# Optimization experiments

Measured on AMD Instinct MI355X. Metric: run time of the kernel, lower is better.

The kernel has to match this reference:

```python
import jax, jax.numpy as jnp
import numpy as np

D = 1024
H = 16
HD = D // H
B = 8
S = 1024


def setup_inputs() -> dict:
    key = jax.random.key(0)
    ks = jax.random.split(key, 12)
    std = 0.02
    inp = {
        "x": jax.random.normal(ks[0], (B, S, D), jnp.float32),
        "rel_pos_enc": jax.random.normal(ks[1], (S, HD), jnp.float32) * std,
        "attention_mask": jax.random.randint(ks[2], (B, S), 0, 2, jnp.int32),
        "Wq": jax.random.normal(ks[3], (D, D), jnp.float32) * std,
        "bq": jnp.zeros((D,), jnp.float32),
        "Wk": jax.random.normal(ks[4], (D, D), jnp.float32) * std,
        "bk": jnp.zeros((D,), jnp.float32),
        "Wv": jax.random.normal(ks[5], (D, D), jnp.float32) * std,
        "bv": jnp.zeros((D,), jnp.float32),
        "Wo": jax.random.normal(ks[6], (D, D), jnp.float32) * std,
        "bo": jnp.zeros((D,), jnp.float32),
    }
    return inp


def reference(x, rel_pos_enc, attention_mask, Wq, bq, Wk, bk, Wv, bv, Wo, bo):
    b, s, d = x.shape
    scale = HD ** -0.5
    # projections + split heads -> [B, H, S, hd]
    q = (x @ Wq + bq).reshape(b, s, H, HD).transpose(0, 2, 1, 3)
    k = (x @ Wk + bk).reshape(b, s, H, HD).transpose(0, 2, 1, 3)
    v = (x @ Wv + bv).reshape(b, s, H, HD).transpose(0, 2, 1, 3)
    # content scores [B,H,S,S]
    scores = jnp.einsum("bhsd,bhtd->bhst", q, k) * scale
    # additive relative-position bias: q . rel_pos_enc[t]  -> [B,H,S,S]
    scores = scores + jnp.einsum("bhsd,td->bhst", q, rel_pos_enc)
    # key-padding mask [B,S] -> [B,1,1,S]
    scores = jnp.where(attention_mask[:, None, None, :] == 0, -jnp.inf, scores)
    attn = jax.nn.softmax(scores, axis=-1)
    ctx = jnp.einsum("bhst,bhtd->bhsd", attn, v)
    ctx = ctx.transpose(0, 2, 1, 3).reshape(b, s, d)
    return ctx @ Wo + bo
```

## Files before the change

### kernel.cpp

```cpp
#include <hip/hip_runtime.h>

#define DD 1024
#define HH 16
#define HDD 64
#define BBATCH 8
#define SS 1024
#define NROW (BBATCH*SS)
#define PSTR 72

typedef _Float16 f16x8 __attribute__((ext_vector_type(8)));
typedef _Float16 f16x4 __attribute__((ext_vector_type(4)));
typedef float    f32x4 __attribute__((ext_vector_type(4)));

__device__ __forceinline__ void async_cp16(const void* g, void* l) {
    __builtin_amdgcn_global_load_lds(
        (const __attribute__((address_space(1))) void*)g,
        (__attribute__((address_space(3))) void*)l, 16, 0, 0);
}

__global__ __launch_bounds__(256) void conv_x_kernel(
    const float* __restrict__ x, _Float16* __restrict__ xh)
{
    size_t i8 = ((size_t)blockIdx.x * 256 + threadIdx.x) * 8;
    float4 v0 = *(const float4*)&x[i8];
    float4 v1 = *(const float4*)&x[i8 + 4];
    float vf[8] = {v0.x, v0.y, v0.z, v0.w, v1.x, v1.y, v1.z, v1.w};
    f16x8 hv;
    #pragma unroll
    for (int c = 0; c < 8; c++) hv[c] = (_Float16)vf[c];
    *(f16x8*)&xh[i8] = hv;
}

__global__ __launch_bounds__(256) void conv_w_kernel(
    const float* __restrict__ Wq, const float* __restrict__ Wk,
    const float* __restrict__ Wv, const float* __restrict__ Wo,
    _Float16* __restrict__ wt, _Float16* __restrict__ wot)
{
    __shared__ float T[64][65];
    const int z = blockIdx.z;
    const float* src = (z == 0) ? Wq : (z == 1) ? Wk : (z == 2) ? Wv : Wo;
    _Float16* dh = (z < 3) ? wt + (size_t)z * 1024 * 1024 : wot;
    const int k0 = blockIdx.x * 64, n0 = blockIdx.y * 64;
    const int tid = threadIdx.x;

    #pragma unroll
    for (int rep = 0; rep < 4; rep++) {
        int e = rep * 256 + tid;
        int kr = e >> 4, nc = (e & 15) * 4;
        *(float4*)&T[kr][nc] = *(const float4*)&src[(size_t)(k0 + kr) * 1024 + n0 + nc];
    }
    __syncthreads();
    #pragma unroll
    for (int rep = 0; rep < 4; rep++) {
        int e = rep * 256 + tid;
        int nr = e >> 4, kc = (e & 15) * 4;
        f16x4 hv;
        #pragma unroll
        for (int c = 0; c < 4; c++) hv[c] = (_Float16)T[kc + c][nr];
        *(f16x4*)&dh[(size_t)(n0 + nr) * 1024 + k0 + kc] = hv;
    }
}

__global__ __launch_bounds__(256) void gemm_f16(
    const _Float16* __restrict__ Ag, const _Float16* __restrict__ Bg,
    const float* __restrict__ b0, const float* __restrict__ b1,
    const float* __restrict__ b2, const float* __restrict__ rel,
    _Float16* __restrict__ oq, _Float16* __restrict__ okh,
    _Float16* __restrict__ ovt, float* __restrict__ dOut, int mode)
{
    __shared__ _Float16 smem[32768];

    const int tid = threadIdx.x;
    const int w = tid >> 6, l = tid & 63;
    const int lane15 = l & 15, quad = l >> 4;
    const int rm = (w >> 1) * 64, cn = (w & 1) * 64;
    const size_t r0 = (size_t)blockIdx.y * 128;
    const size_t n0 = (size_t)blockIdx.x * 128;

    const int srow = tid >> 3;
    const int schp = tid & 7;
    const int sch  = schp ^ (srow & 7);

    f32x4 acc[4][4] = {};

    #pragma unroll
    for (int i = 0; i < 4; i++) {
        int row = i * 32 + srow;
        int s = row * 8 + schp;
        async_cp16(&Ag[(r0 + row) * 1024 + sch * 8], &smem[s * 8]);
        async_cp16(&Bg[(n0 + row) * 1024 + sch * 8], &smem[8192 + s * 8]);
    }
    #pragma unroll
    for (int i = 0; i < 4; i++) {
        int row = i * 32 + srow;
        int s = row * 8 + schp;
        async_cp16(&Ag[(r0 + row) * 1024 + 64 + sch * 8], &smem[16384 + s * 8]);
        async_cp16(&Bg[(n0 + row) * 1024 + 64 + sch * 8], &smem[16384 + 8192 + s * 8]);
    }

    for (int ks = 0; ks < 16; ks++) {
        const _Float16* Ah = smem + (ks & 1) * 16384;
        const _Float16* Bh = Ah + 8192;

        if (ks < 15) asm volatile("s_waitcnt vmcnt(8)" ::: "memory");
        else         asm volatile("s_waitcnt vmcnt(0)" ::: "memory");
        __builtin_amdgcn_sched_barrier(0);
        __builtin_amdgcn_s_barrier();
        __builtin_amdgcn_sched_barrier(0);

        #pragma unroll
        for (int ksub = 0; ksub < 2; ksub++) {
            f16x8 ah[4], bh4[4];
            #pragma unroll
            for (int ii = 0; ii < 4; ii++) {
                int row = rm + ii * 16 + lane15;
                int chp = (ksub * 4 + quad) ^ (row & 7);
                ah[ii] = *(const f16x8*)&Ah[row * 64 + chp * 8];
            }
            #pragma unroll
            for (int jj = 0; jj < 4; jj++) {
                int col = cn + jj * 16 + lane15;
                int chp = (ksub * 4 + quad) ^ (col & 7);
                bh4[jj] = *(const f16x8*)&Bh[col * 64 + chp * 8];
            }
            #pragma unroll
            for (int ii = 0; ii < 4; ii++)
                #pragma unroll
                for (int jj = 0; jj < 4; jj++)
                    acc[ii][jj] = __builtin_amdgcn_mfma_f32_16x16x32_f16(
                        ah[ii], bh4[jj], acc[ii][jj], 0, 0, 0);
        }

        __builtin_amdgcn_sched_barrier(0);
        __builtin_amdgcn_s_barrier();
        __builtin_amdgcn_sched_barrier(0);

        if (ks + 2 < 16) {
            const int kb = (ks + 2) * 64;
            _Float16* An = smem + (ks & 1) * 16384;
            _Float16* Bn = An + 8192;
            #pragma unroll
            for (int i = 0; i < 4; i++) {
                int row = i * 32 + srow;
                int s = row * 8 + schp;
                async_cp16(&Ag[(r0 + row) * 1024 + kb + sch * 8], &An[s * 8]);
                async_cp16(&Bg[(n0 + row) * 1024 + kb + sch * 8], &Bn[s * 8]);
            }
        }
    }

    if (mode == 0) {
        const int z = blockIdx.x >> 3;
        const float* bias = (z == 0) ? b0 : (z == 1) ? b1 : b2;
        const int nbase = (blockIdx.x & 7) * 128 + cn;
        #pragma unroll
        for (int ii = 0; ii < 4; ii++)
            #pragma unroll
            for (int jj = 0; jj < 4; jj++) {
                int nc = nbase + jj * 16 + lane15;
                int hh = nc >> 6, hd = nc & 63;
                float bsv = bias[nc];
                #pragma unroll
                for (int r = 0; r < 4; r++) {
                    int gr = (int)r0 + rm + ii * 16 + quad * 4 + r;
                    int bb = gr >> 10, s = gr & 1023;
                    float val = acc[ii][jj][r] + bsv;
                    size_t hidx = (((size_t)bb * HH + hh) * SS + s) * HDD + hd;
                    if (z == 0) {
                        oq[hidx] = (_Float16)val;
                    } else if (z == 1) {
                        okh[hidx] = (_Float16)(val * 0.125f + rel[s * HDD + hd]);
                    } else {
                        ovt[(((size_t)bb * HH + hh) * HDD + hd) * SS + s] = (_Float16)val;
                    }
                }
            }
    } else {
        #pragma unroll
        for (int ii = 0; ii < 4; ii++)
            #pragma unroll
            for (int jj = 0; jj < 4; jj++) {
                int nc = (int)n0 + cn + jj * 16 + lane15;
                float bsv = b0[nc];
                #pragma unroll
                for (int r = 0; r < 4; r++) {
                    int gr = (int)r0 + rm + ii * 16 + quad * 4 + r;
                    dOut[(size_t)gr * DD + nc] = acc[ii][jj][r] + bsv;
                }
            }
    }
}

__global__ __launch_bounds__(512, 4) void attn_mfma(
    const _Float16* __restrict__ qh, const _Float16* __restrict__ kh,
    const _Float16* __restrict__ vt, const int* __restrict__ mask,
    _Float16* __restrict__ ctx)
{
    __shared__ _Float16 Kbuf[2][64 * PSTR];
    __shared__ _Float16 Vbuf[2][64 * PSTR];
    __shared__ _Float16 Ps[256 * PSTR];
    __shared__ float maddL[1024];

    const int tid = threadIdx.x;
    const int w = tid >> 6, l = tid & 63;
    const int lane15 = l & 15, quad = l >> 4;
    const int id = blockIdx.x;
    const int qt = id >> 7;
    const int bh = id & 127;
    const int b = bh >> 4, h = bh & 15;
    const size_t kbase0 = (size_t)bh * SS;
    const size_t vbase0 = (size_t)bh * HDD;
    const int qrow_blk = qt * 256 + w * 32;

    for (int i = tid; i < 1024; i += 512)
        maddL[i] = (mask[b * SS + i] == 0) ? -1e30f : 0.0f;

    f16x8 qf[2][2];
    #pragma unroll
    for (int g = 0; g < 2; g++)
        #pragma unroll
        for (int ks = 0; ks < 2; ks++)
            qf[g][ks] = *(const f16x8*)&qh[(kbase0 + qrow_blk + g * 16 + lane15) * HDD + ks * 32 + quad * 8];

    f16x8 vone;
    #pragma unroll
    for (int j = 0; j < 8; j++) vone[j] = (lane15 == 0) ? (_Float16)1.0f : (_Float16)0.0f;

    f32x4 O[2][5] = {};

    const int grow = tid >> 3;
    const int gcc  = (tid & 7) * 8;
    const _Float16* kp = &kh[(kbase0 + grow) * HDD + gcc];
    const _Float16* vp = &vt[(vbase0 + grow) * SS + gcc];
    f16x8 kreg = *(const f16x8*)kp;
    f16x8 vreg = *(const f16x8*)vp;

    int p = 0;
    for (int kt = 0; kt < 16; kt++) {
        *(f16x8*)&Kbuf[p][grow * PSTR + gcc] = kreg;
        *(f16x8*)&Vbuf[p][grow * PSTR + gcc] = vreg;
        __syncthreads();

        const int nkt = (kt + 1) & 15;
        kreg = *(const f16x8*)(kp + (size_t)nkt * 64 * HDD);
        vreg = *(const f16x8*)(vp + (size_t)nkt * 64);

        const int t0 = kt * 64;

        #pragma unroll
        for (int nt = 0; nt < 4; nt++) {
            f16x8 kf0 = *(const f16x8*)&Kbuf[p][(nt * 16 + lane15) * PSTR + quad * 8];
            f16x8 kf1 = *(const f16x8*)&Kbuf[p][(nt * 16 + lane15) * PSTR + 32 + quad * 8];
            float madd = maddL[t0 + nt * 16 + lane15] - 3.0f;
            int colp = (nt * 16 + lane15 + 16 * quad) & 63;
            #pragma unroll
            for (int g = 0; g < 2; g++) {
                f32x4 c = {};
                c = __builtin_amdgcn_mfma_f32_16x16x32_f16(qf[g][0], kf0, c, 0, 0, 0);
                c = __builtin_amdgcn_mfma_f32_16x16x32_f16(qf[g][1], kf1, c, 0, 0, 0);
                int rowb = w * 32 + g * 16 + quad * 4;
                #pragma unroll
                for (int r = 0; r < 4; r++)
                    Ps[(rowb + r) * PSTR + colp] = (_Float16)__expf(c[r] + madd);
            }
        }

        const int swz = 16 * (lane15 >> 2);
        #pragma unroll
        for (int ks2 = 0; ks2 < 2; ks2++) {
            int colp = (ks2 * 32 + quad * 8 + swz) & 63;
            f16x8 pf0 = *(const f16x8*)&Ps[(w * 32 + lane15) * PSTR + colp];
            f16x8 pf1 = *(const f16x8*)&Ps[(w * 32 + 16 + lane15) * PSTR + colp];
            #pragma unroll
            for (int nd = 0; nd < 4; nd++) {
                f16x8 vf = *(const f16x8*)&Vbuf[p][(nd * 16 + lane15) * PSTR + ks2 * 32 + quad * 8];
                O[0][nd] = __builtin_amdgcn_mfma_f32_16x16x32_f16(pf0, vf, O[0][nd], 0, 0, 0);
                O[1][nd] = __builtin_amdgcn_mfma_f32_16x16x32_f16(pf1, vf, O[1][nd], 0, 0, 0);
            }
            O[0][4] = __builtin_amdgcn_mfma_f32_16x16x32_f16(pf0, vone, O[0][4], 0, 0, 0);
            O[1][4] = __builtin_amdgcn_mfma_f32_16x16x32_f16(pf1, vone, O[1][4], 0, 0, 0);
        }
        p ^= 1;
    }

    #pragma unroll
    for (int g = 0; g < 2; g++) {
        float linv[4];
        #pragma unroll
        for (int r = 0; r < 4; r++) {
            float lsum = __shfl(O[g][4][r], l & 48, 64);
            linv[r] = 1.0f / lsum;
        }
        #pragma unroll
        for (int nd = 0; nd < 4; nd++) {
            int d = nd * 16 + lane15;
            #pragma unroll
            for (int r = 0; r < 4; r++) {
                int qrow = qt * 256 + w * 32 + g * 16 + quad * 4 + r;
                ctx[((size_t)b * SS + qrow) * DD + h * HDD + d] =
                    (_Float16)(O[g][nd][r] * linv[r]);
            }
        }
    }
}

extern "C" void kernel_launch(void* const* d_in, const int* in_sizes, int n_in,
                              void* d_out, int out_size, void* d_ws, size_t ws_size,
                              hipStream_t stream) {
    const float* x    = (const float*)d_in[0];
    const float* rel  = (const float*)d_in[1];
    const int*   mask = (const int*)d_in[2];
    const float* Wq = (const float*)d_in[3];  const float* bq = (const float*)d_in[4];
    const float* Wk = (const float*)d_in[5];  const float* bk = (const float*)d_in[6];
    const float* Wv = (const float*)d_in[7];  const float* bv = (const float*)d_in[8];
    const float* Wo = (const float*)d_in[9];  const float* bo = (const float*)d_in[10];
    float* out = (float*)d_out;

    const size_t XN = (size_t)NROW * DD;
    char* p = (char*)d_ws;
    _Float16* xh  = (_Float16*)p; p += XN * 2;
    _Float16* wt  = (_Float16*)p; p += (size_t)3072 * 1024 * 2;
    _Float16* wot = (_Float16*)p; p += (size_t)1024 * 1024 * 2;
    _Float16* qhp = (_Float16*)p; p += XN * 2;
    _Float16* khp = (_Float16*)p; p += XN * 2;
    _Float16* vtp = (_Float16*)p; p += XN * 2;
    _Float16* ctx = xh;

    conv_x_kernel<<<dim3((unsigned)(XN / 2048)), 256, 0, stream>>>(x, xh);
    conv_w_kernel<<<dim3(16, 16, 4), 256, 0, stream>>>(Wq, Wk, Wv, Wo, wt, wot);
    gemm_f16<<<dim3(24, 64), 256, 0, stream>>>(
        xh, wt, bq, bk, bv, rel, qhp, khp, vtp, nullptr, 0);
    attn_mfma<<<dim3(512), 512, 0, stream>>>(
        qhp, khp, vtp, mask, ctx);
    gemm_f16<<<dim3(8, 64), 256, 0, stream>>>(
        ctx, wot, bo, nullptr, nullptr, nullptr,
        nullptr, nullptr, nullptr, out, 1);
}
```

Baseline: 277.9 us.

## Pre-swizzle weights into MFMA fragment layout and load B directly to registers

```diff
diff --git a/kernel.cpp b/kernel.cpp
--- a/kernel.cpp
+++ b/kernel.cpp
@@ -57,7 +57,10 @@
         f16x4 hv;
         #pragma unroll
         for (int c = 0; c < 4; c++) hv[c] = (_Float16)T[kc + c][nr];
-        *(f16x4*)&dh[(size_t)(n0 + nr) * 1024 + k0 + kc] = hv;
+        int n = n0 + nr, k = k0 + kc;
+        size_t fa = ((size_t)(n >> 4) * 32 + (k >> 5)) * 512
+                  + (size_t)((n & 15) + 16 * ((k >> 3) & 3)) * 8 + (k & 7);
+        *(f16x4*)&dh[fa] = hv;
     }
 }
 
@@ -68,7 +71,7 @@
     _Float16* __restrict__ oq, _Float16* __restrict__ okh,
     _Float16* __restrict__ ovt, float* __restrict__ dOut, int mode)
 {
-    __shared__ _Float16 smem[32768];
+    __shared__ _Float16 smem[16384];
 
     const int tid = threadIdx.x;
     const int w = tid >> 6, l = tid & 63;
@@ -81,70 +84,81 @@
     const int schp = tid & 7;
     const int sch  = schp ^ (srow & 7);
 
+    const int ntb = ((int)n0 + cn) >> 4;
+
     f32x4 acc[4][4] = {};
-
+    f16x8 bfr[2][4][2];
+
+    #pragma unroll
+    for (int jj = 0; jj < 4; jj++)
+        #pragma unroll
+        for (int kk = 0; kk < 2; kk++)
+            bfr[0][jj][kk] = *(const f16x8*)&Bg[
+                ((size_t)(ntb + jj) * 32 + kk) * 512 + l * 8];
     #pragma unroll
     for (int i = 0; i < 4; i++) {
         int row = i * 32 + srow;
         int s = row * 8 + schp;
         async_cp16(&Ag[(r0 + row) * 1024 + sch * 8], &smem[s * 8]);
-        async_cp16(&Bg[(n0 + row) * 1024 + sch * 8], &smem[8192 + s * 8]);
     }
     #pragma unroll
     for (int i = 0; i < 4; i++) {
         int row = i * 32 + srow;
         int s = row * 8 + schp;
-        async_cp16(&Ag[(r0 + row) * 1024 + 64 + sch * 8], &smem[16384 + s * 8]);
-        async_cp16(&Bg[(n0 + row) * 1024 + 64 + sch * 8], &smem[16384 + 8192 + s * 8]);
-    }
-
-    for (int ks = 0; ks < 16; ks++) {
-        const _Float16* Ah = smem + (ks & 1) * 16384;
-        const _Float16* Bh = Ah + 8192;
-
-        if (ks < 15) asm volatile("s_waitcnt vmcnt(8)" ::: "memory");
-        else         asm volatile("s_waitcnt vmcnt(0)" ::: "memory");
-        __builtin_amdgcn_sched_barrier(0);
-        __builtin_amdgcn_s_barrier();
-        __builtin_amdgcn_sched_barrier(0);
-
-        #pragma unroll
-        for (int ksub = 0; ksub < 2; ksub++) {
-            f16x8 ah[4], bh4[4];
-            #pragma unroll
-            for (int ii = 0; ii < 4; ii++) {
-                int row = rm + ii * 16 + lane15;
-                int chp = (ksub * 4 + quad) ^ (row & 7);
-                ah[ii] = *(const f16x8*)&Ah[row * 64 + chp * 8];
-            }
-            #pragma unroll
-            for (int jj = 0; jj < 4; jj++) {
-                int col = cn + jj * 16 + lane15;
-                int chp = (ksub * 4 + quad) ^ (col & 7);
-                bh4[jj] = *(const f16x8*)&Bh[col * 64 + chp * 8];
-            }
-            #pragma unroll
-            for (int ii = 0; ii < 4; ii++)
+        async_cp16(&Ag[(r0 + row) * 1024 + 64 + sch * 8], &smem[8192 + s * 8]);
+    }
+
+    for (int kt2 = 0; kt2 < 16; kt2 += 2) {
+        #pragma unroll
+        for (int hp = 0; hp < 2; hp++) {
+            const int kt = kt2 + hp;
+            const _Float16* Ah = smem + hp * 8192;
+
+            if (kt < 15) asm volatile("s_waitcnt vmcnt(4)" ::: "memory");
+            else         asm volatile("s_waitcnt vmcnt(0)" ::: "memory");
+            __builtin_amdgcn_sched_barrier(0);
+            __builtin_amdgcn_s_barrier();
+            __builtin_amdgcn_sched_barrier(0);
+
+            if (kt < 15) {
                 #pragma unroll
                 for (int jj = 0; jj < 4; jj++)
-                    acc[ii][jj] = __builtin_amdgcn_mfma_f32_16x16x32_f16(
-                        ah[ii], bh4[jj], acc[ii][jj], 0, 0, 0);
-        }
-
-        __builtin_amdgcn_sched_barrier(0);
-        __builtin_amdgcn_s_barrier();
-        __builtin_amdgcn_sched_barrier(0);
-
-        if (ks + 2 < 16) {
-            const int kb = (ks + 2) * 64;
-            _Float16* An = smem + (ks & 1) * 16384;
-            _Float16* Bn = An + 8192;
-            #pragma unroll
-            for (int i = 0; i < 4; i++) {
-                int row = i * 32 + srow;
-                int s = row * 8 + schp;
-                async_cp16(&Ag[(r0 + row) * 1024 + kb + sch * 8], &An[s * 8]);
-                async_cp16(&Bg[(n0 + row) * 1024 + kb + sch * 8], &Bn[s * 8]);
+                    #pragma unroll
+                    for (int kk = 0; kk < 2; kk++)
+                        bfr[hp ^ 1][jj][kk] = *(const f16x8*)&Bg[
+                            ((size_t)(ntb + jj) * 32 + (kt + 1) * 2 + kk) * 512 + l * 8];
+            }
+
+            #pragma unroll
+            for (int ksub = 0; ksub < 2; ksub++) {
+                f16x8 ah[4];
+                #pragma unroll
+                for (int ii = 0; ii < 4; ii++) {
+                    int row = rm + ii * 16 + lane15;
+                    int chp = (ksub * 4 + quad) ^ (row & 7);
+                    ah[ii] = *(const f16x8*)&Ah[row * 64 + chp * 8];
+                }
+                #pragma unroll
+                for (int ii = 0; ii < 4; ii++)
+                    #pragma unroll
+                    for (int jj = 0; jj < 4; jj++)
+                        acc[ii][jj] = __builtin_amdgcn_mfma_f32_16x16x32_f16(
+                            ah[ii], bfr[hp][jj][ksub], acc[ii][jj], 0, 0, 0);
+            }
+
+            __builtin_amdgcn_sched_barrier(0);
+            __builtin_amdgcn_s_barrier();
+            __builtin_amdgcn_sched_barrier(0);
+
+            if (kt + 2 < 16) {
+                const int kb = (kt + 2) * 64;
+                _Float16* An = smem + hp * 8192;
+                #pragma unroll
+                for (int i = 0; i < 4; i++) {
+                    int row = i * 32 + srow;
+                    int s = row * 8 + schp;
+                    async_cp16(&Ag[(r0 + row) * 1024 + kb + sch * 8], &An[s * 8]);
+                }
             }
         }
     }
```

Measured after the change: 289.6 us. +4.2%, slower.
